# Optimization experiments

Hardware: AMD Instinct MI355X
Metric: run time of the kernel (lower is better)

The kernel has to match this reference:

```python
import jax, jax.numpy as jnp
import numpy as np
from jax import lax

K = 5  # up_kernel_size

def nearest_up2(x):
    # PyTorch F.interpolate(scale_factor=2) default mode='nearest': out[i]=in[i//2]
    return jnp.repeat(jnp.repeat(x, 2, axis=2), 2, axis=3)

def conv1x1(x, W, b=None):
    # x: [B,C,H,W], W: [O,C]
    y = jnp.einsum('bchw,oc->bohw', x, W)
    if b is not None:
        y = y + b[None, :, None, None]
    return y

def depthwise3x3(x, W, b):
    # x: [B,25,H,W], W: [25,1,3,3] (OIHW with groups=25)
    y = lax.conv_general_dilated(x, W, window_strides=(1, 1), padding='SAME',
                                 feature_group_count=x.shape[1],
                                 dimension_numbers=('NCHW', 'OIHW', 'NCHW'))
    return y + b[None, :, None, None]

def carafe(de, kernels):
    # de: [B,C,H,W]; kernels: [B,K*K,2H,2W], softmax-normalized over channel dim
    B, C, H, Wd = de.shape
    r = K // 2
    de_p = jnp.pad(de, ((0, 0), (0, 0), (r, r), (r, r)))
    # patches[b,k,c,h,w] = de neighborhood, k = dy*K+dx  -> [B,25,C,H,W]
    patches = jnp.stack([de_p[:, :, dy:dy + H, dx:dx + Wd]
                         for dy in range(K) for dx in range(K)], axis=1)
    # kernels[b,k,2h+s,2w+t] -> [B,25,H,2,W,2]; source pixel is (i//2, j//2)
    kr = kernels.reshape(B, K * K, H, 2, Wd, 2)
    out = jnp.einsum('bkchw,bkhswt->bchswt', patches, kr)
    return out.reshape(B, C, 2 * H, 2 * Wd)

def setup_inputs() -> dict:
    key = jax.random.key(0)
    ks = jax.random.split(key, 8)
    B, C, H, W = 4, 256, 64, 64
    en = jax.random.normal(ks[0], (B, C, 2 * H, 2 * W), dtype=jnp.float32)
    de = jax.random.normal(ks[1], (B, C, H, W), dtype=jnp.float32)
    s = 1.0 / np.sqrt(C)
    W_gate = jax.random.uniform(ks[2], (1, C), jnp.float32, -s, s)
    b_gate = jnp.zeros((1,), jnp.float32)
    W_ce = jax.random.uniform(ks[3], (K * K, C), jnp.float32, -s, s)
    b_ce = jnp.zeros((K * K,), jnp.float32)
    W_cd = jax.random.uniform(ks[4], (K * K, C), jnp.float32, -s, s)
    W_dw = jax.random.uniform(ks[5], (K * K, 1, 3, 3), jnp.float32, -0.33, 0.33)
    b_dw = jnp.zeros((K * K,), jnp.float32)
    return {'en': en, 'de': de, 'W_gate': W_gate, 'b_gate': b_gate,
            'W_ce': W_ce, 'b_ce': b_ce, 'W_cd': W_cd, 'W_dw': W_dw, 'b_dw': b_dw}

def reference(en, de, W_gate, b_gate, W_ce, b_ce, W_cd, W_dw, b_dw):
    # gate generator
    gate = jax.nn.sigmoid(nearest_up2(conv1x1(de, W_gate, b_gate)))  # [B,1,2H,2W]
    # kernel generator (SemiShiftDepthWise)
    enc = conv1x1(en, W_ce, b_ce)      # [B,25,2H,2W]
    dec = conv1x1(de, W_cd)            # [B,25,H,W]
    raw = depthwise3x3(enc, W_dw, b_dw) + nearest_up2(depthwise3x3(dec, W_dw, b_dw))
    kernels = jax.nn.softmax(raw, axis=1)
    return gate * en + (1.0 - gate) * carafe(de, kernels)
```

## Files before the change

### kernel.cpp

```cpp
#include <hip/hip_runtime.h>


typedef unsigned short u16;
typedef unsigned int u32;

#define NB 4
#define NC 256
#define NH 64
#define NW 64
#define NH2 128
#define NW2 128

#define OFF_WG   0
#define OFF_BG   256
#define OFF_WCE  272
#define OFF_BCE  6672
#define OFF_WCD  6704
#define OFF_WDW  13104
#define OFF_BDW  13330
#define OFF_FLAG 13356

#define OFF_GATE 16384
#define OFF_KB   32768
#define OFF_ENC  851968
#define OFF_DEC  2490368
#define OFF_DET  851968
#define OFF_P1   851968
#define FULL_NEED_BYTES 12877824ull

#define NGATE 16384
#define NDEC  20480
#define NENC  122880
#define NKBF  532480

__device__ __forceinline__ float bf2f(u16 u){ return __uint_as_float(((u32)u) << 16); }
__device__ __forceinline__ u16 f2bf(float f){
  u32 x = __float_as_uint(f);
  return (u16)((x + 0x7fffu + ((x >> 16) & 1u)) >> 16);
}
__device__ __forceinline__ float ldin(const void* p, int i, bool f32){
  return f32 ? ((const float*)p)[i] : bf2f(((const u16*)p)[i]);
}

__global__ __launch_bounds__(256) void k_detect(const void* de_raw, float* ws){
  __shared__ int cnt;
  if (threadIdx.x == 0) cnt = 0;
  __syncthreads();
  int c = 0;
#pragma unroll
  for (int s = 0; s < 2; s++) {
    int i = (threadIdx.x + s * 256) * 2;
    u16 u = ((const u16*)de_raw)[i];
    int e = (u >> 7) & 0xff;
    if (e >= 0x70 && e <= 0x82) c++;
  }
  atomicAdd(&cnt, c);
  __syncthreads();
  if (threadIdx.x == 0) ws[OFF_FLAG] = (cnt < 256) ? 1.0f : 0.0f;
}

__global__ __launch_bounds__(256) void k_prep(const void* Wg, const void* bg,
    const void* Wce, const void* bce, const void* Wcd, const void* Wdw, const void* bdw,
    float* ws){
  bool f = ws[OFF_FLAG] != 0.f;
  int i = threadIdx.x + blockIdx.x * 256;
  if (i < 6400) {
    ws[OFF_WCE + i] = ldin(Wce, i, f);
    ws[OFF_WCD + i] = ldin(Wcd, i, f);
    if (i < 256) ws[OFF_WG + i] = ldin(Wg, i, f);
    if (i < 1)   ws[OFF_BG + i] = ldin(bg, i, f);
    if (i < 25)  ws[OFF_BCE + i] = ldin(bce, i, f);
    if (i < 225) ws[OFF_WDW + i] = ldin(Wdw, i, f);
    if (i < 25)  ws[OFF_BDW + i] = ldin(bdw, i, f);
  }
}


__global__ __launch_bounds__(256) void o1a_dec_gate(const void* de, float* ws){
  __shared__ float red[4][26][64];
  bool f = ws[OFF_FLAG] != 0.f;
  int b = blockIdx.x >> 7;
  int rem = blockIdx.x & 127;
  int h = rem >> 1;
  int chunk = rem & 1;
  int g = threadIdx.x >> 6;
  int w = threadIdx.x & 63;
  int c0 = __builtin_amdgcn_readfirstlane(chunk * 128 + g * 32);
  float acc[26];
#pragma unroll
  for (int o = 0; o < 26; o++) acc[o] = 0.f;
  int idx = ((b * NC + c0) * NH + h) * NW + w;
  for (int ci = 0; ci < 32; ci += 8) {
    float v0 = ldin(de, idx,            f);
    float v1 = ldin(de, idx + 1 * 4096, f);
    float v2 = ldin(de, idx + 2 * 4096, f);
    float v3 = ldin(de, idx + 3 * 4096, f);
    float v4 = ldin(de, idx + 4 * 4096, f);
    float v5 = ldin(de, idx + 5 * 4096, f);
    float v6 = ldin(de, idx + 6 * 4096, f);
    float v7 = ldin(de, idx + 7 * 4096, f);
    idx += 8 * 4096;
    int c = c0 + ci;
    acc[25] += ws[OFF_WG + c] * v0 + ws[OFF_WG + c + 1] * v1
             + ws[OFF_WG + c + 2] * v2 + ws[OFF_WG + c + 3] * v3
             + ws[OFF_WG + c + 4] * v4 + ws[OFF_WG + c + 5] * v5
             + ws[OFF_WG + c + 6] * v6 + ws[OFF_WG + c + 7] * v7;
#pragma unroll
    for (int k = 0; k < 25; k++) {
      const float* wk = ws + OFF_WCD + k * 256 + c;
      acc[k] += wk[0] * v0 + wk[1] * v1 + wk[2] * v2 + wk[3] * v3
              + wk[4] * v4 + wk[5] * v5 + wk[6] * v6 + wk[7] * v7;
    }
  }
#pragma unroll
  for (int o = 0; o < 26; o++) red[g][o][w] = acc[o];
  __syncthreads();
  for (int item = threadIdx.x; item < 26 * 64; item += 256) {
    int o = item >> 6; int ww = item & 63;
    float s = red[0][o][ww] + red[1][o][ww] + red[2][o][ww] + red[3][o][ww];
    ws[OFF_P1 + (((chunk * NB + b) * 26 + o) << 12) + (h << 6) + ww] = s;
  }
}

__global__ __launch_bounds__(256) void o1b_reduce(float* ws){
  int i = blockIdx.x * 256 + threadIdx.x;
  int b = i / (26 * 4096);
  int r = i - b * 26 * 4096;
  int o = r >> 12;
  int pix = r & 4095;
  float s = ws[OFF_P1 + (((0 * NB + b) * 26 + o) << 12) + pix]
          + ws[OFF_P1 + (((1 * NB + b) * 26 + o) << 12) + pix];
  if (o < 25)
    ws[OFF_DEC + ((b * 25 + o) << 12) + pix] = s;
  else {
    float z = s + ws[OFF_BG];
    ws[OFF_GATE + (b << 12) + pix] = 1.f / (1.f + __expf(-z));
  }
}

__global__ __launch_bounds__(256) void o2_det(const void* de, float* ws){
  __shared__ float tile[64][65];
  bool f = ws[OFF_FLAG] != 0.f;
  u16* det = (u16*)(ws + OFF_DET);
  int b = blockIdx.x / 272;
  int r = blockIdx.x % 272;
  int p = r >> 2;
  int c0 = (r & 3) << 6;
  int h = p - 2;
  bool hv = (h >= 0 && h < NH);
  for (int item = threadIdx.x; item < 64 * 64; item += 256) {
    int cl = item >> 6, w = item & 63;
    float v = hv ? ldin(de, ((b * NC + c0 + cl) * NH + h) * NW + w, f) : 0.f;
    tile[w][cl] = v;
  }
  __syncthreads();
  u16* dst = det + ((b * 68 + p) * 68) * NC + c0;
  for (int item = threadIdx.x; item < 68 * 64; item += 256) {
    int q = item >> 6, cl = item & 63;
    int w = q - 2;
    float v = (w >= 0 && w < NW) ? tile[w][cl] : 0.f;
    dst[q * NC + cl] = f2bf(v);
  }
}

__global__ __launch_bounds__(256) void o3_enc(const void* en, float* ws){
  __shared__ float red[4][25][64];
  bool f = ws[OFF_FLAG] != 0.f;
  int b = blockIdx.x >> 8;
  int rem = blockIdx.x & 255;
  int y = rem >> 1;
  int xs = (rem & 1) << 6;
  int g = threadIdx.x >> 6;
  int xl = threadIdx.x & 63;
  int c0 = __builtin_amdgcn_readfirstlane(g * 64);
  float acc[25];
#pragma unroll
  for (int k = 0; k < 25; k++) acc[k] = 0.f;
  int idx = ((b * NC + c0) * NH2 + y) * NW2 + xs + xl;
  for (int ci = 0; ci < 64; ci += 8) {
    float v0 = ldin(en, idx,             f);
    float v1 = ldin(en, idx + 1 * 16384, f);
    float v2 = ldin(en, idx + 2 * 16384, f);
    float v3 = ldin(en, idx + 3 * 16384, f);
    float v4 = ldin(en, idx + 4 * 16384, f);
    float v5 = ldin(en, idx + 5 * 16384, f);
    float v6 = ldin(en, idx + 6 * 16384, f);
    float v7 = ldin(en, idx + 7 * 16384, f);
    idx += 8 * 16384;
    int c = c0 + ci;
#pragma unroll
    for (int k = 0; k < 25; k++) {
      const float* wk = ws + OFF_WCE + k * 256 + c;
      acc[k] += wk[0] * v0 + wk[1] * v1 + wk[2] * v2 + wk[3] * v3
              + wk[4] * v4 + wk[5] * v5 + wk[6] * v6 + wk[7] * v7;
    }
  }
#pragma unroll
  for (int k = 0; k < 25; k++) red[g][k][xl] = acc[k];
  __syncthreads();
  for (int item = threadIdx.x; item < 25 * 64; item += 256) {
    int k = item >> 6; int xx = item & 63;
    float s = red[0][k][xx] + red[1][k][xx] + red[2][k][xx] + red[3][k][xx]
            + ws[OFF_BCE + k];
    ws[OFF_ENC + ((b * 25 + k) * NH2 + y) * NW2 + xs + xx] = s;
  }
}

__global__ __launch_bounds__(256) void o4_kernels(float* ws){
  __shared__ float red[25][64];
  int b = blockIdx.x >> 8;
  int rem = blockIdx.x & 255;
  int y = rem >> 1;
  int xs = (rem & 1) << 6;
  int tg = __builtin_amdgcn_readfirstlane(threadIdx.x >> 6);
  int xl = threadIdx.x & 63;
  int x = xs + xl;
  int h = y >> 1, w = x >> 1;
  const float* enc = ws + OFF_ENC + (b * 25) * NH2 * NW2;
  const float* dec = ws + OFF_DEC + (b * 25) * NH * NW;

  for (int k = tg; k < 25; k += 4) {
    float s = 2.f * ws[OFF_BDW + k];
#pragma unroll
    for (int u = 0; u < 3; u++) {
      int yy = y + u - 1, hh = h + u - 1;
      bool yok = (yy >= 0 && yy < NH2);
      bool hok = (hh >= 0 && hh < NH);
#pragma unroll
      for (int v = 0; v < 3; v++) {
        int xx = x + v - 1, w2 = w + v - 1;
        float wd = ws[OFF_WDW + k * 9 + u * 3 + v];
        if (yok && xx >= 0 && xx < NW2)
          s += enc[(k * NH2 + yy) * NW2 + xx] * wd;
        if (hok && w2 >= 0 && w2 < NW)
          s += dec[(k * NH + hh) * NW + w2] * wd;
      }
    }
    red[k][xl] = s;
  }
  __syncthreads();

  if (threadIdx.x < 64) {
    int t = threadIdx.x;
    int xp = xs + t;
    float m = -1e30f;
#pragma unroll
    for (int k = 0; k < 25; k++) m = fmaxf(m, red[k][t]);
    float sum = 0.f;
#pragma unroll
    for (int k = 0; k < 25; k++) {
      float e = __expf(red[k][t] - m);
      red[k][t] = e;
      sum += e;
    }
    float inv = 1.f / sum;
    int st = ((y & 1) << 1) + (xp & 1);
    int wp = xp >> 1;
    u16* kbu = (u16*)(ws + OFF_KB);
    u16* dst = kbu + ((b * NH + h) * NW + wp) * 100 + st;
#pragma unroll
    for (int k = 0; k < 25; k++) dst[k * 4] = f2bf(red[k][t] * inv);
  }
}

__global__ __launch_bounds__(256) void o5_final(const void* en, float* ws, float* out){
  __shared__ u16 stag[32][260];
  bool f = ws[OFF_FLAG] != 0.f;
  const u16* det = (const u16*)(ws + OFF_DET);
  const u16* kbu = (const u16*)(ws + OFF_KB);
  const float* gate = ws + OFF_GATE;

  int bi = blockIdx.x;
  int xcd = bi & 7;
  int slot = bi >> 3;
  int s = slot & 1;
  int pid = ((slot >> 1) << 3) | xcd;
  int b = pid >> 8;
  int rem = pid & 255;
  int h = rem >> 2;
  int w0b = (rem & 3) * 16;
  int wave = threadIdx.x >> 6;
  int lane = threadIdx.x & 63;
  int c4 = lane * 4;

  for (int i = 0; i < 4; i++) {
    int wu = __builtin_amdgcn_readfirstlane(w0b + wave * 4 + i);
    const u16* kp = kbu + ((b * NH + h) * NW + wu) * 100 + s * 2;
    float acc[2][4];
#pragma unroll
    for (int t = 0; t < 2; t++)
#pragma unroll
      for (int j = 0; j < 4; j++) acc[t][j] = 0.f;

#pragma unroll
    for (int dy = 0; dy < 5; dy++) {
      const u16* dp = det + (((b * 68 + h + dy) * 68 + wu) * NC) + c4;
#pragma unroll
      for (int dx = 0; dx < 5; dx++) {
        ushort4 uv = *(const ushort4*)(dp + dx * NC);
        float v0 = bf2f(uv.x), v1 = bf2f(uv.y), v2 = bf2f(uv.z), v3 = bf2f(uv.w);
        u32 kk = *(const u32*)(kp + (dy * 5 + dx) * 4);
        float k0 = bf2f((u16)(kk & 0xffffu));
        float k1 = bf2f((u16)(kk >> 16));
        acc[0][0] += k0 * v0; acc[0][1] += k0 * v1; acc[0][2] += k0 * v2; acc[0][3] += k0 * v3;
        acc[1][0] += k1 * v0; acc[1][1] += k1 * v1; acc[1][2] += k1 * v2; acc[1][3] += k1 * v3;
      }
    }
    int xl = (wave * 4 + i) * 2;
#pragma unroll
    for (int t = 0; t < 2; t++) {
      ushort4 pv;
      pv.x = f2bf(acc[t][0]); pv.y = f2bf(acc[t][1]);
      pv.z = f2bf(acc[t][2]); pv.w = f2bf(acc[t][3]);
      *(ushort4*)&stag[xl + t][c4] = pv;
    }
  }
  __syncthreads();

  int xp = threadIdx.x & 31;
  int cb = (threadIdx.x >> 5) * 2;
  int x = w0b * 2 + xp;
  int wpix = w0b + (xp >> 1);
  int y = 2 * h + s;
  float g = gate[(b * NH + h) * NW + wpix];
  float gi = 1.f - g;
#pragma unroll
  for (int pass = 0; pass < 16; pass++) {
    int c = cb + pass * 16;
    u32 rr = *(const u32*)&stag[xp][c];
    float cr0 = bf2f((u16)(rr & 0xffffu));
    float cr1 = bf2f((u16)(rr >> 16));
    int eidx = ((b * NC + c) * NH2 + y) * NW2 + x;
    float e0 = ldin(en, eidx, f);
    float e1 = ldin(en, eidx + NH2 * NW2, f);
    __builtin_nontemporal_store(g * e0 + gi * cr0, &out[eidx]);
    __builtin_nontemporal_store(g * e1 + gi * cr1, &out[eidx + NH2 * NW2]);
  }
}


__global__ __launch_bounds__(256) void kA_gate(const void* de, float* ws, int b){
  bool f = ws[OFF_FLAG] != 0.f;
  int idx = blockIdx.x * 256 + threadIdx.x;
  int h = idx >> 6, w = idx & 63;
  float s = ws[OFF_BG];
  for (int c = 0; c < NC; c++)
    s += ldin(de, ((b * NC + c) * NH + h) * NW + w, f) * ws[OFF_WG + c];
  ws[NGATE + idx] = 1.f / (1.f + __expf(-s));
}

__global__ __launch_bounds__(256) void kB_dec(const void* de, float* ws, int b){
  bool f = ws[OFF_FLAG] != 0.f;
  int idx = blockIdx.x * 256 + threadIdx.x;
  int h = idx >> 6, w = idx & 63;
  float acc[25];
#pragma unroll
  for (int k = 0; k < 25; k++) acc[k] = 0.f;
  for (int c = 0; c < NC; c++) {
    float v = ldin(de, ((b * NC + c) * NH + h) * NW + w, f);
#pragma unroll
    for (int k = 0; k < 25; k++) acc[k] += v * ws[OFF_WCD + k * 256 + c];
  }
#pragma unroll
  for (int k = 0; k < 25; k++)
    ws[NDEC + (k * NH + h) * NW + w] = acc[k];
}

__global__ __launch_bounds__(256) void kC_enc(const void* en, float* ws, int b){
  bool f = ws[OFF_FLAG] != 0.f;
  int idx = blockIdx.x * 256 + threadIdx.x;
  int y = idx >> 7, x = idx & 127;
  float acc[25];
#pragma unroll
  for (int k = 0; k < 25; k++) acc[k] = 0.f;
  for (int c = 0; c < NC; c++) {
    float v = ldin(en, ((b * NC + c) * NH2 + y) * NW2 + x, f);
#pragma unroll
    for (int k = 0; k < 25; k++) acc[k] += v * ws[OFF_WCE + k * 256 + c];
  }
#pragma unroll
  for (int k = 0; k < 25; k++)
    ws[NENC + (k * NH2 + y) * NW2 + x] = acc[k] + ws[OFF_BCE + k];
}

__global__ __launch_bounds__(256) void kD_kern(float* ws){
  int idx = blockIdx.x * 256 + threadIdx.x;
  int y = idx >> 7, x = idx & 127;
  int h = y >> 1, w = x >> 1;
  float raw[25];
#pragma unroll
  for (int k = 0; k < 25; k++) {
    float s = 2.f * ws[OFF_BDW + k];
#pragma unroll
    for (int u = 0; u < 3; u++) {
      int yy = y + u - 1, hh = h + u - 1;
#pragma unroll
      for (int v = 0; v < 3; v++) {
        int xx = x + v - 1, ww = w + v - 1;
        float wd = ws[OFF_WDW + k * 9 + u * 3 + v];
        if (yy >= 0 && yy < NH2 && xx >= 0 && xx < NW2)
          s += ws[NENC + (k * NH2 + yy) * NW2 + xx] * wd;
        if (hh >= 0 && hh < NH && ww >= 0 && ww < NW)
          s += ws[NDEC + (k * NH + hh) * NW + ww] * wd;
      }
    }
    raw[k] = s;
  }
  float m = raw[0];
#pragma unroll
  for (int k = 1; k < 25; k++) m = fmaxf(m, raw[k]);
  float sum = 0.f;
#pragma unroll
  for (int k = 0; k < 25; k++) { raw[k] = __expf(raw[k] - m); sum += raw[k]; }
  float inv = 1.f / sum;
  float* dst = ws + NKBF + idx * 25;
#pragma unroll
  for (int k = 0; k < 25; k++) dst[k] = raw[k] * inv;
}

__global__ __launch_bounds__(256) void kE_out(const void* en, const void* de,
    const float* ws, float* out, int b){
  bool f = ws[OFF_FLAG] != 0.f;
  int idx = blockIdx.x * 256 + threadIdx.x;
  int c = idx >> 14;
  int y = (idx >> 7) & 127;
  int x = idx & 127;
  int h = y >> 1, w = x >> 1;
  const float* kb = ws + NKBF + (y * NW2 + x) * 25;
  float acc = 0.f;
#pragma unroll
  for (int dy = 0; dy < 5; dy++) {
    int hh = h + dy - 2;
    if (hh < 0 || hh >= NH) continue;
#pragma unroll
    for (int dx = 0; dx < 5; dx++) {
      int ww = w + dx - 2;
      if (ww < 0 || ww >= NW) continue;
      acc += ldin(de, ((b * NC + c) * NH + hh) * NW + ww, f) * kb[dy * 5 + dx];
    }
  }
  float g = ws[NGATE + h * NW + w];
  float e = ldin(en, ((b * NC + c) * NH2 + y) * NW2 + x, f);
  out[((b * NC + c) * NH2 + y) * NW2 + x] = g * e + (1.f - g) * acc;
}

static const void* find_by_size(void* const* d_in, const int* in_sizes, int n_in,
                                int want, int skip, const void* fb){
  int seen = 0;
  for (int i = 0; i < n_in; i++)
    if (in_sizes[i] == want) {
      if (seen == skip) return d_in[i];
      seen++;
    }
  return fb;
}

extern "C" void kernel_launch(void* const* d_in, const int* in_sizes, int n_in,
                              void* d_out, int out_size, void* d_ws, size_t ws_size,
                              hipStream_t stream) {
  (void)out_size;
  const void* en  = find_by_size(d_in, in_sizes, n_in, 4*256*128*128, 0, d_in[0]);
  const void* de  = find_by_size(d_in, in_sizes, n_in, 4*256*64*64,   0, d_in[1]);
  const void* Wg  = find_by_size(d_in, in_sizes, n_in, 256,           0, d_in[2]);
  const void* bg  = find_by_size(d_in, in_sizes, n_in, 1,             0, d_in[3]);
  const void* Wce = find_by_size(d_in, in_sizes, n_in, 6400,          0, d_in[4]);
  const void* bce = find_by_size(d_in, in_sizes, n_in, 25,            0, d_in[5]);
  const void* Wcd = find_by_size(d_in, in_sizes, n_in, 6400,          1, d_in[6]);
  const void* Wdw = find_by_size(d_in, in_sizes, n_in, 225,           0, d_in[7]);
  const void* bdw = find_by_size(d_in, in_sizes, n_in, 25,            1, d_in[8]);
  float* ws = (float*)d_ws;
  float* out = (float*)d_out;

  hipLaunchKernelGGL(k_detect, dim3(1), dim3(256), 0, stream, de, ws);
  hipLaunchKernelGGL(k_prep, dim3(25), dim3(256), 0, stream,
                     Wg, bg, Wce, bce, Wcd, Wdw, bdw, ws);

  if (ws_size >= FULL_NEED_BYTES) {
    hipLaunchKernelGGL(o1a_dec_gate, dim3(NB * NH * 2),     dim3(256), 0, stream, de, ws);
    hipLaunchKernelGGL(o1b_reduce,   dim3(1664),            dim3(256), 0, stream, ws);
    hipLaunchKernelGGL(o3_enc,       dim3(NB * NH2 * 2),    dim3(256), 0, stream, en, ws);
    hipLaunchKernelGGL(o4_kernels,   dim3(NB * NH2 * 2),    dim3(256), 0, stream, ws);
    hipLaunchKernelGGL(o2_det,       dim3(NB * 68 * 4),     dim3(256), 0, stream, de, ws);
    hipLaunchKernelGGL(o5_final,     dim3(NB * NH * 4 * 2), dim3(256), 0, stream, en, ws, out);
  } else {
    for (int b = 0; b < NB; b++) {
      hipLaunchKernelGGL(kA_gate, dim3(16),    dim3(256), 0, stream, de, ws, b);
      hipLaunchKernelGGL(kB_dec,  dim3(16),    dim3(256), 0, stream, de, ws, b);
      hipLaunchKernelGGL(kC_enc,  dim3(64),    dim3(256), 0, stream, en, ws, b);
      hipLaunchKernelGGL(kD_kern, dim3(64),    dim3(256), 0, stream, ws);
      hipLaunchKernelGGL(kE_out,  dim3(16384), dim3(256), 0, stream, en, de, ws, out, b);
    }
  }
}
```

Measured before the change: 249.3 us.

## Reuse decoder row loads across four pixels and use packed FMA in CARAFE

The CARAFE reassembly loop now computes all four adjacent output pixels of a wave together. Each dy row loads 8 neighbouring decoder columns once and reuses them across the overlapping 5-wide windows, which cuts global loads from 100 to 40 per row set. The multiply-accumulate uses inline v_pk_fma_f32 with op_sel broadcasting of the kernel weight, and bf16 is unpacked with shifts and masks. This raises register pressure (32 accumulators plus 16 cached words), which could lower occupancy.

```diff
diff --git a/kernel.cpp b/kernel.cpp
--- a/kernel.cpp
+++ b/kernel.cpp
@@ -3,6 +3,7 @@
 
 typedef unsigned short u16;
 typedef unsigned int u32;
+typedef float v2f __attribute__((ext_vector_type(2)));
 
 #define NB 4
 #define NC 256
@@ -283,35 +284,59 @@
   int lane = threadIdx.x & 63;
   int c4 = lane * 4;
 
+  int wu0 = __builtin_amdgcn_readfirstlane(w0b + wave * 4);
+  const u16* kp0 = kbu + ((b * NH + h) * NW + wu0) * 100 + s * 2;
+
+  v2f acc[4][2][2];
+#pragma unroll
+  for (int i = 0; i < 4; i++)
+#pragma unroll
+    for (int t = 0; t < 2; t++)
+#pragma unroll
+      for (int p = 0; p < 2; p++) { acc[i][t][p].x = 0.f; acc[i][t][p].y = 0.f; }
+
+#pragma unroll
+  for (int dy = 0; dy < 5; dy++) {
+    const u16* dp = det + (((b * 68 + h + dy) * 68 + wu0) * NC) + c4;
+    u32 wlo[8], whi[8];
+#pragma unroll
+    for (int j = 0; j < 8; j++) {
+      uint2 dv = *(const uint2*)(dp + j * NC);
+      wlo[j] = dv.x; whi[j] = dv.y;
+    }
+#pragma unroll
+    for (int i = 0; i < 4; i++) {
+#pragma unroll
+      for (int dx = 0; dx < 5; dx++) {
+        int j = i + dx;
+        u32 kk = *(const u32*)(kp0 + i * 100 + (dy * 5 + dx) * 4);
+        v2f kp2, vA, vB;
+        kp2.x = __uint_as_float(kk << 16);
+        kp2.y = __uint_as_float(kk & 0xffff0000u);
+        vA.x = __uint_as_float(wlo[j] << 16);
+        vA.y = __uint_as_float(wlo[j] & 0xffff0000u);
+        vB.x = __uint_as_float(whi[j] << 16);
+        vB.y = __uint_as_float(whi[j] & 0xffff0000u);
+        asm("v_pk_fma_f32 %0, %1, %2, %0 op_sel:[0,0,0] op_sel_hi:[0,1,1]"
+            : "+v"(acc[i][0][0]) : "v"(kp2), "v"(vA));
+        asm("v_pk_fma_f32 %0, %1, %2, %0 op_sel:[0,0,0] op_sel_hi:[0,1,1]"
+            : "+v"(acc[i][0][1]) : "v"(kp2), "v"(vB));
+        asm("v_pk_fma_f32 %0, %1, %2, %0 op_sel:[1,0,0] op_sel_hi:[1,1,1]"
+            : "+v"(acc[i][1][0]) : "v"(kp2), "v"(vA));
+        asm("v_pk_fma_f32 %0, %1, %2, %0 op_sel:[1,0,0] op_sel_hi:[1,1,1]"
+            : "+v"(acc[i][1][1]) : "v"(kp2), "v"(vB));
+      }
+    }
+  }
+
+#pragma unroll
   for (int i = 0; i < 4; i++) {
-    int wu = __builtin_amdgcn_readfirstlane(w0b + wave * 4 + i);
-    const u16* kp = kbu + ((b * NH + h) * NW + wu) * 100 + s * 2;
-    float acc[2][4];
-#pragma unroll
-    for (int t = 0; t < 2; t++)
-#pragma unroll
-      for (int j = 0; j < 4; j++) acc[t][j] = 0.f;
-
-#pragma unroll
-    for (int dy = 0; dy < 5; dy++) {
-      const u16* dp = det + (((b * 68 + h + dy) * 68 + wu) * NC) + c4;
-#pragma unroll
-      for (int dx = 0; dx < 5; dx++) {
-        ushort4 uv = *(const ushort4*)(dp + dx * NC);
-        float v0 = bf2f(uv.x), v1 = bf2f(uv.y), v2 = bf2f(uv.z), v3 = bf2f(uv.w);
-        u32 kk = *(const u32*)(kp + (dy * 5 + dx) * 4);
-        float k0 = bf2f((u16)(kk & 0xffffu));
-        float k1 = bf2f((u16)(kk >> 16));
-        acc[0][0] += k0 * v0; acc[0][1] += k0 * v1; acc[0][2] += k0 * v2; acc[0][3] += k0 * v3;
-        acc[1][0] += k1 * v0; acc[1][1] += k1 * v1; acc[1][2] += k1 * v2; acc[1][3] += k1 * v3;
-      }
-    }
     int xl = (wave * 4 + i) * 2;
 #pragma unroll
     for (int t = 0; t < 2; t++) {
       ushort4 pv;
-      pv.x = f2bf(acc[t][0]); pv.y = f2bf(acc[t][1]);
-      pv.z = f2bf(acc[t][2]); pv.w = f2bf(acc[t][3]);
+      pv.x = f2bf(acc[i][t][0].x); pv.y = f2bf(acc[i][t][0].y);
+      pv.z = f2bf(acc[i][t][1].x); pv.w = f2bf(acc[i][t][1].y);
       *(ushort4*)&stag[xl + t][c4] = pv;
     }
   }
```

Result: faster. 239.9 us (-3.8%).
